# Kernel tuning notes

Measured on AMD Instinct MI355X. Metric: run time of the kernel, lower is better.

The kernel has to match this reference:

```python
import jax, jax.numpy as jnp
import numpy as np

C = 256; CM = 8; MAXI = 100; NCLS = 80
KP = (CM + 2) * CM + CM + CM * CM + CM + CM + 1  # 169 dynamic-kernel params

def _ln(x, g, b, eps=1e-5):
    m = x.mean(-1, keepdims=True)
    v = ((x - m) ** 2).mean(-1, keepdims=True)
    return g * (x - m) * jax.lax.rsqrt(v + eps) + b

def _mlp(x, hw, hb, lng, lnb, fw, fb):
    # torchvision MLP: [Linear -> LayerNorm -> SiLU] * n_hidden -> Linear
    for i in range(hw.shape[0]):
        x = jax.nn.silu(_ln(x @ hw[i] + hb[i], lng[i], lnb[i]))
    return x @ fw + fb

def _conv1x1_bn(x, w, s, b):
    # 1x1 conv (no bias) + inference-mode BatchNorm folded into per-channel affine
    y = jnp.einsum('bchw,oc->bohw', x, w)
    return y * s[None, :, None, None] + b[None, :, None, None]

def _grid(h, w):
    # normalized cell-center coordinates, (x, y) order, shape [h, w, 2]
    ys = (jnp.arange(h, dtype=jnp.float32) + 0.5) / h
    xs = (jnp.arange(w, dtype=jnp.float32) + 0.5) / w
    return jnp.stack([jnp.broadcast_to(xs[None, :], (h, w)),
                      jnp.broadcast_to(ys[:, None], (h, w))], axis=-1)

def setup_inputs() -> dict:
    key = jax.random.key(0)
    ks = iter(jax.random.split(key, 40))
    nrm = lambda shape, s=0.02: s * jax.random.normal(next(ks), shape, jnp.float32)
    B = 4
    inp = {
        'x0': jax.random.normal(next(ks), (B, 3, 512, 512), jnp.float32),
        'x1': jax.random.normal(next(ks), (B, 64, 256, 256), jnp.float32),
        'x2': jax.random.normal(next(ks), (B, 128, 128, 128), jnp.float32),
        'x3': jax.random.normal(next(ks), (B, 256, 64, 64), jnp.float32),
        'x4': jax.random.normal(next(ks), (B, 512, 32, 32), jnp.float32),
        'x5': jax.random.normal(next(ks), (B, 1024, 16, 16), jnp.float32),
        'lat3_w': nrm((C, 256)), 'lat3_s': jnp.ones((C,)), 'lat3_b': jnp.zeros((C,)),
        'lat4_w': nrm((C, 512)), 'lat4_s': jnp.ones((C,)), 'lat4_b': jnp.zeros((C,)),
        'lat5_w': nrm((C, 1024)), 'lat5_s': jnp.ones((C,)), 'lat5_b': jnp.zeros((C,)),
        'mlat_w': nrm((C, 256)), 'mlat_s': jnp.ones((C,)), 'mlat_b': jnp.zeros((C,)),
        'mhead_w': nrm((CM, C, 3, 3)), 'mhead_s': jnp.ones((CM,)), 'mhead_b': jnp.zeros((CM,)),
        'loc_hw': nrm((4, C, C)), 'loc_hb': jnp.zeros((4, C)), 'loc_lng': jnp.ones((4, C)), 'loc_lnb': jnp.zeros((4, C)),
        'loc_fw': nrm((C, 1)), 'loc_fb': -5.0 * jnp.ones((1,)),
        'cls_hw': nrm((4, C, C)), 'cls_hb': jnp.zeros((4, C)), 'cls_lng': jnp.ones((4, C)), 'cls_lnb': jnp.zeros((4, C)),
        'cls_fw': nrm((C, NCLS)), 'cls_fb': jnp.zeros((NCLS,)),
        'ker_hw': nrm((4, C, C)), 'ker_hb': jnp.zeros((4, C)), 'ker_lng': jnp.ones((4, C)), 'ker_lnb': jnp.zeros((4, C)),
        'ker_fw': nrm((C, KP)), 'ker_fb': jnp.zeros((KP,)),
    }
    return inp

def reference(x0, x1, x2, x3, x4, x5,
              lat3_w, lat3_s, lat3_b, lat4_w, lat4_s, lat4_b, lat5_w, lat5_s, lat5_b,
              mlat_w, mlat_s, mlat_b, mhead_w, mhead_s, mhead_b,
              loc_hw, loc_hb, loc_lng, loc_lnb, loc_fw, loc_fb,
              cls_hw, cls_hb, cls_lng, cls_lnb, cls_fw, cls_fb,
              ker_hw, ker_hb, ker_lng, ker_lnb, ker_fw, ker_fb):
    B, _, H, W = x0.shape
    lvls = [(x3, lat3_w, lat3_s, lat3_b), (x4, lat4_w, lat4_s, lat4_b), (x5, lat5_w, lat5_s, lat5_b)]
    feats = [_conv1x1_bn(x, w, s, b) for (x, w, s, b) in lvls]
    flat = jnp.concatenate([f.reshape(B, C, -1).transpose(0, 2, 1) for f in feats], axis=1)  # [B, L, C]
    loc_logits = _mlp(flat, loc_hw, loc_hb, loc_lng, loc_lnb, loc_fw, loc_fb)[..., 0]       # [B, L]
    top_vals, top_idx = jax.lax.top_k(loc_logits, MAXI)
    scores = jax.nn.sigmoid(top_vals)
    num_instances = (scores > 0.5).sum(axis=1)
    gfeat = jnp.take_along_axis(flat, top_idx[:, :, None], axis=1)  # [B, I, C]
    # mask branch
    mf = _conv1x1_bn(x3, mlat_w, mlat_s, mlat_b)
    mf = jax.lax.conv_general_dilated(mf, mhead_w, (1, 1), 'SAME', dimension_numbers=('NCHW', 'OIHW', 'NCHW'))
    mf = jax.nn.silu(mf * mhead_s[None, :, None, None] + mhead_b[None, :, None, None])  # [B, CM, h3, w3]
    h3, w3 = x3.shape[2], x3.shape[3]
    offs_flat = jnp.concatenate([_grid(x.shape[2], x.shape[3]).reshape(-1, 2) for x in (x3, x4, x5)], axis=0)
    offs = offs_flat[top_idx]                                # [B, I, 2]
    grid = _grid(h3, w3).transpose(2, 0, 1)                  # [2, h3, w3]
    grid = grid[None, None] - offs[:, :, :, None, None]      # [B, I, 2, h, w]
    mfi = jnp.broadcast_to(mf[:, None], (B, MAXI, CM, h3, w3))
    feats_i = jnp.concatenate([mfi, grid], axis=2)           # [B, I, CM+2, h, w]
    dyn = _mlp(gfeat, ker_hw, ker_hb, ker_lng, ker_lnb, ker_fw, ker_fb)  # [B, I, KP]
    c = CM
    o = (c + 2) * c
    w1 = dyn[..., :o].reshape(B, MAXI, c + 2, c)
    b1 = dyn[..., o:o + c].reshape(B, MAXI, c, 1, 1); o += c
    w2 = dyn[..., o:o + c * c].reshape(B, MAXI, c, c); o += c * c
    b2 = dyn[..., o:o + c].reshape(B, MAXI, c, 1, 1); o += c
    w3 = dyn[..., o:o + c].reshape(B, MAXI, c, 1); o += c
    b3 = dyn[..., o:].reshape(B, MAXI, 1, 1, 1)
    m = jax.nn.silu(jnp.einsum('bichw,bicd->bidhw', feats_i, w1) + b1)
    m = jax.nn.silu(jnp.einsum('bichw,bicd->bidhw', m, w2) + b2)
    m = jnp.einsum('bichw,bicd->bidhw', m, w3) + b3
    masks = jax.nn.sigmoid(m[:, :, 0])                       # [B, I, h3, w3]
    classes = jnp.argmax(_mlp(gfeat, cls_hw, cls_hb, cls_lng, cls_lnb, cls_fw, cls_fb), axis=-1)
    masks = jax.image.resize(masks, (B, MAXI, H, W), method='bilinear', antialias=False)
    return (num_instances, scores, classes, masks)
```

## Files before the change

kernel.cpp:

```cpp
#include <hip/hip_runtime.h>
#include <hip/hip_bf16.h>
#include <math.h>

#define DEVI __device__ __forceinline__

constexpr int LTOT  = 5376;
constexpr int NINST = 100;
constexpr int NCLS  = 80;
constexpr int KPAR  = 169;

DEVI float waveAllSum(float v) {
#pragma unroll
  for (int s = 32; s > 0; s >>= 1) v += __shfl_xor(v, s, 64);
  return v;
}
DEVI float siluf(float x) { return x / (1.0f + expf(-x)); }
DEVI float sigmf(float x) { return 1.0f / (1.0f + expf(-x)); }

__global__ __launch_bounds__(256) void wtrans(
    const float* __restrict__ w3, const float* __restrict__ w4,
    const float* __restrict__ w5, const float* __restrict__ wm,
    float* __restrict__ wt3, float* __restrict__ wt4,
    float* __restrict__ wt5, float* __restrict__ wtm)
{
  __shared__ float t[64][65];
  const int bid = blockIdx.x;
  const float* src; float* dst; int K, rel;
  if (bid < 16)       { src = w3; dst = wt3; K = 256;  rel = bid; }
  else if (bid < 48)  { src = w4; dst = wt4; K = 512;  rel = bid - 16; }
  else if (bid < 112) { src = w5; dst = wt5; K = 1024; rel = bid - 48; }
  else                { src = wm; dst = wtm; K = 256;  rel = bid - 112; }
  const int ctiles = K >> 6;
  const int ot = rel / ctiles, ct = rel % ctiles;
  const int o0 = ot * 64, c0 = ct * 64;
  const int tid = threadIdx.x;
#pragma unroll
  for (int s = 0; s < 16; ++s) {
    const int e = tid + 256*s;
    const int r = e >> 6, c = e & 63;
    t[r][c] = src[(long)(o0 + r)*K + c0 + c];
  }
  __syncthreads();
#pragma unroll
  for (int s = 0; s < 16; ++s) {
    const int e = tid + 256*s;
    const int q = e >> 6, p = e & 63;
    dst[(long)(c0 + q)*256 + o0 + p] = t[p][q];
  }
}

__global__ __launch_bounds__(256) void lateral_main(
    const float* __restrict__ x3, const float* __restrict__ x4, const float* __restrict__ x5,
    const float* __restrict__ wt3, const float* __restrict__ s3, const float* __restrict__ b3,
    const float* __restrict__ wt4, const float* __restrict__ s4, const float* __restrict__ b4,
    const float* __restrict__ wt5, const float* __restrict__ s5, const float* __restrict__ b5,
    const float* __restrict__ wtm, const float* __restrict__ sm, const float* __restrict__ bm,
    float* __restrict__ flat, float* __restrict__ mlatb)
{
  __shared__ float xs[32][36];
  __shared__ float ws[32][256];
  const int tid = threadIdx.x;
  const int rg = tid >> 6, cg = tid & 63;
  const int bid = blockIdx.x;
  const float *x, *wt, *sc, *bi;
  int K, P, b, p0, baseL = 0; bool tomlat = false;
  if (bid < 512)       { x=x3; wt=wt3; sc=s3; bi=b3; K=256;  P=4096; b=bid>>7;  p0=(bid&127)*32; }
  else if (bid < 1024) { const int rel=bid-512;  x=x3; wt=wtm; sc=sm; bi=bm; K=256;  P=4096; b=rel>>7; p0=(rel&127)*32; tomlat=true; }
  else if (bid < 1152) { const int rel=bid-1024; x=x4; wt=wt4; sc=s4; bi=b4; K=512;  P=1024; b=rel>>5; p0=(rel&31)*32; baseL=4096; }
  else                 { const int rel=bid-1152; x=x5; wt=wt5; sc=s5; bi=b5; K=1024; P=256;  b=rel>>3; p0=(rel&7)*32;  baseL=5120; }
  const float* xb = x + (long)b * K * P;
  float acc[8][4] = {};
  const int nkb = K >> 5;
  for (int kb = 0; kb < nkb; ++kb) {
    __syncthreads();
#pragma unroll
    for (int s = 0; s < 4; ++s) {
      const int e = tid + 256*s;
      const int kk = e >> 5, px = e & 31;
      xs[kk][px] = xb[(long)(kb*32 + kk)*P + p0 + px];
    }
    {
      const float4* w4p = reinterpret_cast<const float4*>(wt + (kb << 13));
#pragma unroll
      for (int q = 0; q < 8; ++q) {
        const int c = tid + (q << 8);
        *reinterpret_cast<float4*>(&ws[c >> 6][4*(c & 63)]) = w4p[c];
      }
    }
    __syncthreads();
#pragma unroll
    for (int kk = 0; kk < 32; ++kk) {
      const float4 a0 = *reinterpret_cast<const float4*>(&xs[kk][8*rg]);
      const float4 a1 = *reinterpret_cast<const float4*>(&xs[kk][8*rg+4]);
      const float ar[8] = {a0.x,a0.y,a0.z,a0.w,a1.x,a1.y,a1.z,a1.w};
      const float4 wv = *reinterpret_cast<const float4*>(&ws[kk][4*cg]);
#pragma unroll
      for (int i = 0; i < 8; ++i) {
        acc[i][0] += ar[i]*wv.x; acc[i][1] += ar[i]*wv.y;
        acc[i][2] += ar[i]*wv.z; acc[i][3] += ar[i]*wv.w;
      }
    }
  }
  const float4 sA = *reinterpret_cast<const float4*>(&sc[4*cg]);
  const float4 bA = *reinterpret_cast<const float4*>(&bi[4*cg]);
  if (!tomlat) {
#pragma unroll
    for (int i = 0; i < 8; ++i) {
      const float4 ov = { acc[i][0]*sA.x+bA.x, acc[i][1]*sA.y+bA.y,
                          acc[i][2]*sA.z+bA.z, acc[i][3]*sA.w+bA.w };
      *reinterpret_cast<float4*>(&flat[((long)b*LTOT + baseL + p0 + 8*rg + i)*256 + 4*cg]) = ov;
    }
  } else {
#pragma unroll
    for (int j = 0; j < 4; ++j) {
      const float sj = (&sA.x)[j], bj = (&bA.x)[j];
      const float4 o0 = { acc[0][j]*sj+bj, acc[1][j]*sj+bj, acc[2][j]*sj+bj, acc[3][j]*sj+bj };
      const float4 o1 = { acc[4][j]*sj+bj, acc[5][j]*sj+bj, acc[6][j]*sj+bj, acc[7][j]*sj+bj };
      float* mb = &mlatb[((long)b*256 + 4*cg + j)*4096 + p0 + 8*rg];
      *reinterpret_cast<float4*>(mb) = o0;
      *reinterpret_cast<float4*>(mb + 4) = o1;
    }
  }
}

__global__ __launch_bounds__(256) void loc4(
    const float* __restrict__ in, const float* __restrict__ hw,
    const float* __restrict__ hb, const float* __restrict__ lng, const float* __restrict__ lnb,
    const float* __restrict__ fw, const float* __restrict__ fb, float* __restrict__ logits)
{
  __shared__ float xs[256][36];
  __shared__ float wsm[16][256];
  const int tid = threadIdx.x;
  const int rg = tid >> 6, cg = tid & 63;
  const long r0 = (long)blockIdx.x * 32;
#pragma unroll
  for (int s = 0; s < 8; ++s) {
    const int e = tid + 256*s;
    const int row = e >> 6, q = e & 63;
    const float4 v = *reinterpret_cast<const float4*>(&in[(r0 + row)*256 + 4*q]);
    const int pc = 8*((row >> 3) ^ (q & 3)) + (row & 7);
#pragma unroll
    for (int j = 0; j < 4; ++j) xs[4*q+j][pc] = (&v.x)[j];
  }
  float ov[8][4];
  for (int L = 0; L < 4; ++L) {
    const float* w = hw + L*65536;
    float acc[8][4] = {};
    for (int kb = 0; kb < 16; ++kb) {
      __syncthreads();
      const float4* w4 = reinterpret_cast<const float4*>(w + (kb << 12));
#pragma unroll
      for (int q = 0; q < 4; ++q) {
        const int c = tid + (q << 8);
        *reinterpret_cast<float4*>(&wsm[c>>6][4*(c&63)]) = w4[c];
      }
      __syncthreads();
#pragma unroll
      for (int kk = 0; kk < 16; ++kk) {
        const int k = (kb << 4) + kk;
        const int col = 8*(rg ^ ((k >> 2) & 3));
        const float4 a0 = *reinterpret_cast<const float4*>(&xs[k][col]);
        const float4 a1 = *reinterpret_cast<const float4*>(&xs[k][col+4]);
        const float4 wv = *reinterpret_cast<const float4*>(&wsm[kk][4*cg]);
        const float ar[8] = {a0.x,a0.y,a0.z,a0.w,a1.x,a1.y,a1.z,a1.w};
#pragma unroll
        for (int i = 0; i < 8; ++i) {
          acc[i][0] += ar[i]*wv.x; acc[i][1] += ar[i]*wv.y;
          acc[i][2] += ar[i]*wv.z; acc[i][3] += ar[i]*wv.w;
        }
      }
    }
    const float4 hb4 = *reinterpret_cast<const float4*>(&hb[L*256 + 4*cg]);
    const float4 g4  = *reinterpret_cast<const float4*>(&lng[L*256 + 4*cg]);
    const float4 lb4 = *reinterpret_cast<const float4*>(&lnb[L*256 + 4*cg]);
#pragma unroll
    for (int i = 0; i < 8; ++i) {
      const float y0 = acc[i][0]+hb4.x, y1 = acc[i][1]+hb4.y;
      const float y2 = acc[i][2]+hb4.z, y3 = acc[i][3]+hb4.w;
      const float m = waveAllSum(y0+y1+y2+y3) * (1.0f/256.0f);
      const float d0=y0-m, d1=y1-m, d2=y2-m, d3=y3-m;
      const float var = waveAllSum(d0*d0+d1*d1+d2*d2+d3*d3) * (1.0f/256.0f);
      const float rs = rsqrtf(var + 1e-5f);
      ov[i][0] = siluf(g4.x*d0*rs + lb4.x);
      ov[i][1] = siluf(g4.y*d1*rs + lb4.y);
      ov[i][2] = siluf(g4.z*d2*rs + lb4.z);
      ov[i][3] = siluf(g4.w*d3*rs + lb4.w);
    }
    __syncthreads();
    if (L < 3) {
      const int colb = 8*(rg ^ (cg & 3));
#pragma unroll
      for (int j = 0; j < 4; ++j) {
        const float4 t0 = {ov[0][j], ov[1][j], ov[2][j], ov[3][j]};
        const float4 t1 = {ov[4][j], ov[5][j], ov[6][j], ov[7][j]};
        *reinterpret_cast<float4*>(&xs[4*cg+j][colb])   = t0;
        *reinterpret_cast<float4*>(&xs[4*cg+j][colb+4]) = t1;
      }
    }
  }
  const float4 fw4 = *reinterpret_cast<const float4*>(&fw[4*cg]);
  const float fbv = fb[0];
#pragma unroll
  for (int i = 0; i < 8; ++i) {
    float d = ov[i][0]*fw4.x + ov[i][1]*fw4.y + ov[i][2]*fw4.z + ov[i][3]*fw4.w;
    d = waveAllSum(d);
    if (cg == 0) logits[r0 + 8*rg + i] = d + fbv;
  }
}

__global__ __launch_bounds__(256) void topk_gather(
    const float* __restrict__ logits, const float* __restrict__ flat,
    int* __restrict__ topi, float* __restrict__ gfeat,
    float* __restrict__ dout)
{
  __shared__ float sv[LTOT];
  __shared__ float rv[4];
  __shared__ int   ri[4];
  __shared__ int   sidx[NINST];
  const int b = blockIdx.x, tid = threadIdx.x;
  for (int l = tid; l < LTOT; l += 256) sv[l] = logits[b*LTOT + l];
  __syncthreads();
  int cnt = 0;
  for (int t = 0; t < NINST; ++t) {
    float bv = -INFINITY; int bidx = 0x7fffffff;
    for (int l = tid; l < LTOT; l += 256) {
      const float v = sv[l];
      if (v > bv) { bv = v; bidx = l; }
    }
#pragma unroll
    for (int s = 32; s > 0; s >>= 1) {
      const float v2 = __shfl_xor(bv, s, 64);
      const int   i2 = __shfl_xor(bidx, s, 64);
      if (v2 > bv || (v2 == bv && i2 < bidx)) { bv = v2; bidx = i2; }
    }
    if ((tid & 63) == 0) { rv[tid >> 6] = bv; ri[tid >> 6] = bidx; }
    __syncthreads();
    if (tid == 0) {
      bv = rv[0]; bidx = ri[0];
#pragma unroll
      for (int q = 1; q < 4; ++q)
        if (rv[q] > bv || (rv[q] == bv && ri[q] < bidx)) { bv = rv[q]; bidx = ri[q]; }
      sidx[t] = bidx; topi[b*NINST + t] = bidx;
      dout[4 + b*NINST + t] = sigmf(bv);
      if (bv > 0.0f) ++cnt;
      sv[bidx] = -INFINITY;
    }
    __syncthreads();
  }
  if (tid == 0) dout[b] = (float)cnt;
  for (int t = 0; t < NINST; ++t) {
    const int ix = sidx[t];
    gfeat[((long)b*NINST + t)*256 + tid] = flat[((long)b*LTOT + ix)*256 + tid];
  }
}

__global__ __launch_bounds__(256) void clsker4(
    const float* __restrict__ gfeat, float* __restrict__ h2,
    const float* __restrict__ chw, const float* __restrict__ chb,
    const float* __restrict__ cg_, const float* __restrict__ cb_,
    const float* __restrict__ khw, const float* __restrict__ khb,
    const float* __restrict__ kg_, const float* __restrict__ kb_)
{
  __shared__ float xs[256][12];
  __shared__ float wsm[16][256];
  const int tid = threadIdx.x;
  const int rg = tid >> 6, cg = tid & 63;
  const bool ker = blockIdx.x >= 50;
  const int r0 = (ker ? (blockIdx.x - 50) : blockIdx.x) * 8;
  const int outr0 = r0 + (ker ? 400 : 0);
  const float* hw = ker ? khw : chw;
  const float* hb = ker ? khb : chb;
  const float* g_ = ker ? kg_ : cg_;
  const float* lb = ker ? kb_ : cb_;
#pragma unroll
  for (int s = 0; s < 2; ++s) {
    const int e = tid + 256*s;
    const int row = e >> 6, q = e & 63;
    const float4 v = *reinterpret_cast<const float4*>(&gfeat[(long)(r0 + row)*256 + 4*q]);
    const int pc = 2*((row >> 1) ^ (q & 3)) + (row & 1);
#pragma unroll
    for (int j = 0; j < 4; ++j) xs[4*q+j][pc] = (&v.x)[j];
  }
  float ov[2][4];
  for (int L = 0; L < 4; ++L) {
    const float* w = hw + L*65536;
    float acc[2][4] = {};
    for (int kb = 0; kb < 16; ++kb) {
      __syncthreads();
      const float4* w4 = reinterpret_cast<const float4*>(w + (kb << 12));
#pragma unroll
      for (int q = 0; q < 4; ++q) {
        const int c = tid + (q << 8);
        *reinterpret_cast<float4*>(&wsm[c>>6][4*(c&63)]) = w4[c];
      }
      __syncthreads();
#pragma unroll
      for (int kk = 0; kk < 16; ++kk) {
        const int k = (kb << 4) + kk;
        const float2 av = *reinterpret_cast<const float2*>(&xs[k][2*(rg ^ ((k >> 2) & 3))]);
        const float4 wv = *reinterpret_cast<const float4*>(&wsm[kk][4*cg]);
        acc[0][0] += av.x*wv.x; acc[0][1] += av.x*wv.y; acc[0][2] += av.x*wv.z; acc[0][3] += av.x*wv.w;
        acc[1][0] += av.y*wv.x; acc[1][1] += av.y*wv.y; acc[1][2] += av.y*wv.z; acc[1][3] += av.y*wv.w;
      }
    }
    const float4 hb4 = *reinterpret_cast<const float4*>(&hb[L*256 + 4*cg]);
    const float4 g4  = *reinterpret_cast<const float4*>(&g_[L*256 + 4*cg]);
    const float4 lb4 = *reinterpret_cast<const float4*>(&lb[L*256 + 4*cg]);
#pragma unroll
    for (int i = 0; i < 2; ++i) {
      const float y0 = acc[i][0]+hb4.x, y1 = acc[i][1]+hb4.y;
      const float y2 = acc[i][2]+hb4.z, y3 = acc[i][3]+hb4.w;
      const float m = waveAllSum(y0+y1+y2+y3) * (1.0f/256.0f);
      const float d0=y0-m, d1=y1-m, d2=y2-m, d3=y3-m;
      const float var = waveAllSum(d0*d0+d1*d1+d2*d2+d3*d3) * (1.0f/256.0f);
      const float rs = rsqrtf(var + 1e-5f);
      ov[i][0] = siluf(g4.x*d0*rs + lb4.x);
      ov[i][1] = siluf(g4.y*d1*rs + lb4.y);
      ov[i][2] = siluf(g4.z*d2*rs + lb4.z);
      ov[i][3] = siluf(g4.w*d3*rs + lb4.w);
    }
    __syncthreads();
    if (L < 3) {
      const int pc = 2*(rg ^ (cg & 3));
#pragma unroll
      for (int j = 0; j < 4; ++j) {
        const float2 t = {ov[0][j], ov[1][j]};
        *reinterpret_cast<float2*>(&xs[4*cg+j][pc]) = t;
      }
    }
  }
#pragma unroll
  for (int i = 0; i < 2; ++i) {
    const float4 o = {ov[i][0], ov[i][1], ov[i][2], ov[i][3]};
    *reinterpret_cast<float4*>(&h2[(long)(outr0 + 2*rg + i)*256 + 4*cg]) = o;
  }
}

__global__ __launch_bounds__(256) void heads(
    const float* __restrict__ h2, const float* __restrict__ cfw, const float* __restrict__ cfb,
    const float* __restrict__ kfw, const float* __restrict__ kfb,
    float* __restrict__ dout, float* __restrict__ dyn)
{
  __shared__ float xr[256];
  __shared__ float lv[NCLS];
  const int bid = blockIdx.x, tid = threadIdx.x;
  xr[tid] = h2[(long)bid*256 + tid];
  __syncthreads();
  if (bid < 400) {
    if (tid < NCLS) {
      float a0=0.f, a1=0.f, a2=0.f, a3=0.f;
      for (int k = 0; k < 256; k += 4) {
        a0 += xr[k+0]*cfw[(k+0)*NCLS + tid];
        a1 += xr[k+1]*cfw[(k+1)*NCLS + tid];
        a2 += xr[k+2]*cfw[(k+2)*NCLS + tid];
        a3 += xr[k+3]*cfw[(k+3)*NCLS + tid];
      }
      lv[tid] = (a0+a1) + (a2+a3) + cfb[tid];
    }
    __syncthreads();
    if (tid == 0) {
      float bv = lv[0]; int bi2 = 0;
      for (int o = 1; o < NCLS; ++o) if (lv[o] > bv) { bv = lv[o]; bi2 = o; }
      dout[404 + bid] = (float)bi2;
    }
  } else {
    if (tid < KPAR) {
      float a0=0.f, a1=0.f, a2=0.f, a3=0.f;
      for (int k = 0; k < 256; k += 4) {
        a0 += xr[k+0]*kfw[(k+0)*KPAR + tid];
        a1 += xr[k+1]*kfw[(k+1)*KPAR + tid];
        a2 += xr[k+2]*kfw[(k+2)*KPAR + tid];
        a3 += xr[k+3]*kfw[(k+3)*KPAR + tid];
      }
      dyn[(long)(bid-400)*KPAR + tid] = (a0+a1) + (a2+a3) + kfb[tid];
    }
  }
}

__global__ __launch_bounds__(256) void conv3(
    const float* __restrict__ mlat, const float* __restrict__ mw,
    float* __restrict__ partial)
{
  const int bid = blockIdx.x;
  const int cc = bid & 7;
  const int tile = (bid >> 3) & 15;
  const int b = bid >> 7;
  const int y0 = (tile >> 2)*16, x0 = (tile & 3)*16;
  const int tid = threadIdx.x;
  const int ly = tid >> 4, lx = tid & 15;
  __shared__ float til[2][18][19];
  __shared__ float wch[8][32][12];
  for (int e = tid; e < 2304; e += 256) {
    const int o = e / 288, rem = e % 288;
    const int c = rem / 9, qq = rem - c*9;
    wch[o][c][qq] = mw[((o*256) + cc*32 + c)*9 + qq];
  }
  int lofs[3], gofs[3], chn[3]; bool vld[3], has[3];
  float* tf = &til[0][0][0];
#pragma unroll
  for (int s = 0; s < 3; ++s) {
    const int e = tid + 256*s;
    has[s] = (e < 648);
    lofs[s] = 0; gofs[s] = 0; chn[s] = 0; vld[s] = false;
    if (has[s]) {
      const int ch = (e >= 324) ? 1 : 0;
      const int pos = e - ch*324;
      const int iy = pos / 18, ix = pos - iy*18;
      const int gy = y0 - 1 + iy, gx = x0 - 1 + ix;
      vld[s] = (gy >= 0 && gy < 64 && gx >= 0 && gx < 64);
      lofs[s] = ch*342 + iy*19 + ix;
      gofs[s] = gy*64 + gx;
      chn[s] = ch;
    }
  }
  const float* xbase = mlat + ((long)b*256 + cc*32)*4096;
  float acc[8] = {};
  for (int r = 0; r < 16; ++r) {
    __syncthreads();
#pragma unroll
    for (int s = 0; s < 3; ++s)
      if (has[s]) tf[lofs[s]] = vld[s] ? xbase[(long)(2*r + chn[s])*4096 + gofs[s]] : 0.f;
    __syncthreads();
#pragma unroll
    for (int ch = 0; ch < 2; ++ch) {
      const int c = 2*r + ch;
      float t[9];
#pragma unroll
      for (int dy = 0; dy < 3; ++dy)
#pragma unroll
        for (int dx = 0; dx < 3; ++dx) t[dy*3+dx] = til[ch][ly+dy][lx+dx];
#pragma unroll
      for (int o = 0; o < 8; ++o) {
        const float4 wa = *reinterpret_cast<const float4*>(&wch[o][c][0]);
        const float4 wb = *reinterpret_cast<const float4*>(&wch[o][c][4]);
        const float w8 = wch[o][c][8];
        acc[o] += t[0]*wa.x + t[1]*wa.y + t[2]*wa.z + t[3]*wa.w
                + t[4]*wb.x + t[5]*wb.y + t[6]*wb.z + t[7]*wb.w + t[8]*w8;
      }
    }
  }
  const long pbase = (((long)b*8 + cc)*8)*4096 + (y0+ly)*64 + (x0+lx);
#pragma unroll
  for (int o = 0; o < 8; ++o) partial[pbase + (long)o*4096] = acc[o];
}

__global__ __launch_bounds__(256) void mhead_fin(
    const float* __restrict__ partial, const float* __restrict__ s,
    const float* __restrict__ bi, float* __restrict__ mhead)
{
  const int idx = blockIdx.x*256 + threadIdx.x;
  const int p = idx & 4095;
  const int o = (idx >> 12) & 7;
  const int b = idx >> 15;
  float v = 0.f;
#pragma unroll
  for (int cc = 0; cc < 8; ++cc) v += partial[(((long)b*8 + cc)*8 + o)*4096 + p];
  v = v*s[o] + bi[o];
  mhead[idx] = siluf(v);
}

__global__ __launch_bounds__(256) void mask_fused(
    const float* __restrict__ dyn, const int* __restrict__ topi,
    const float* __restrict__ mhead, float* __restrict__ dout)
{
  __shared__ float msrc[18][64];
  __shared__ float dd[KPAR];
  __shared__ float so[2];
  const int bid = blockIdx.x;
  const int inst = bid >> 2, q = bid & 3;
  const int tid = threadIdx.x;
  if (tid < KPAR) dd[tid] = dyn[(long)inst*KPAR + tid];
  if (tid == 0) {
    const int l = topi[inst];
    float ox, oy;
    if (l < 4096)      { ox = ((l & 63) + 0.5f)*(1.f/64.f); oy = ((l >> 6) + 0.5f)*(1.f/64.f); }
    else if (l < 5120) { const int t = l - 4096; ox = ((t & 31) + 0.5f)*(1.f/32.f); oy = ((t >> 5) + 0.5f)*(1.f/32.f); }
    else               { const int t = l - 5120; ox = ((t & 15) + 0.5f)*(1.f/16.f); oy = ((t >> 4) + 0.5f)*(1.f/16.f); }
    so[0] = ox; so[1] = oy;
  }
  __syncthreads();
  const float ox = so[0], oy = so[1];
  const int b = inst / NINST;
  const float* mh = mhead + (long)b*8*4096;
  const int r0s = 16*q - 1;
  for (int e = tid; e < 1152; e += 256) {
    const int r = e >> 6, x = e & 63;
    int sy = r0s + r; sy = sy < 0 ? 0 : (sy > 63 ? 63 : sy);
    const int p = sy*64 + x;
    float f[10];
#pragma unroll
    for (int c = 0; c < 8; ++c) f[c] = mh[c*4096 + p];
    f[8] = (x + 0.5f)*(1.f/64.f) - ox;
    f[9] = (sy + 0.5f)*(1.f/64.f) - oy;
    float m1[8];
#pragma unroll
    for (int d = 0; d < 8; ++d) {
      float t = dd[80 + d];
#pragma unroll
      for (int c = 0; c < 10; ++c) t += f[c]*dd[c*8 + d];
      m1[d] = siluf(t);
    }
    float m2[8];
#pragma unroll
    for (int d = 0; d < 8; ++d) {
      float t = dd[152 + d];
#pragma unroll
      for (int c = 0; c < 8; ++c) t += m1[c]*dd[88 + c*8 + d];
      m2[d] = siluf(t);
    }
    float o = dd[168];
#pragma unroll
    for (int c = 0; c < 8; ++c) o += m2[c]*dd[160 + c];
    msrc[r][x] = sigmf(o);
  }
  __syncthreads();
  const int j4 = tid & 127;
  const int half = tid >> 7;
  const int ix0 = (j4 & 1) ? (j4 >> 1) : (j4 >> 1) - 1;
  const int xlo = ix0 < 0 ? 0 : ix0;
  const int xhi = (ix0 + 1 > 63) ? 63 : ix0 + 1;
  float fx[4];
#pragma unroll
  for (int m = 0; m < 4; ++m) {
    const int x = 4*j4 + m;
    const float tx = (x + 0.5f)*0.125f - 0.5f;
    fx[m] = tx - (float)ix0;
  }
  float* dbase = dout + 804 + ((long)inst << 18);
  for (int it = 0; it < 64; ++it) {
    const int yy = 2*it + half;
    const int y = 128*q + yy;
    const float ty = (y + 0.5f)*0.125f - 0.5f;
    const float fyf = floorf(ty);
    const int iy0 = (int)fyf;
    const float fy = ty - fyf;
    const int r0 = iy0 - r0s;
    const float L0 = msrc[r0][xlo],   R0 = msrc[r0][xhi];
    const float L1 = msrc[r0+1][xlo], R1 = msrc[r0+1][xhi];
    const float L = L0 + (L1 - L0)*fy;
    const float R = R0 + (R1 - R0)*fy;
    const float4 ovv = { L + (R - L)*fx[0], L + (R - L)*fx[1],
                         L + (R - L)*fx[2], L + (R - L)*fx[3] };
    *reinterpret_cast<float4*>(&dbase[((long)y << 9) + (j4 << 2)]) = ovv;
  }
}

extern "C" void kernel_launch(void* const* d_in, const int* in_sizes, int n_in,
                              void* d_out, int out_size, void* d_ws, size_t ws_size,
                              hipStream_t stream)
{
  (void)in_sizes; (void)n_in; (void)out_size; (void)ws_size;
  const float* x3      = (const float*)d_in[3];
  const float* x4      = (const float*)d_in[4];
  const float* x5      = (const float*)d_in[5];
  const float* lat3_w  = (const float*)d_in[6];
  const float* lat3_s  = (const float*)d_in[7];
  const float* lat3_b  = (const float*)d_in[8];
  const float* lat4_w  = (const float*)d_in[9];
  const float* lat4_s  = (const float*)d_in[10];
  const float* lat4_b  = (const float*)d_in[11];
  const float* lat5_w  = (const float*)d_in[12];
  const float* lat5_s  = (const float*)d_in[13];
  const float* lat5_b  = (const float*)d_in[14];
  const float* mlat_w  = (const float*)d_in[15];
  const float* mlat_s  = (const float*)d_in[16];
  const float* mlat_b  = (const float*)d_in[17];
  const float* mhead_w = (const float*)d_in[18];
  const float* mhead_s = (const float*)d_in[19];
  const float* mhead_b = (const float*)d_in[20];
  const float* loc_hw  = (const float*)d_in[21];
  const float* loc_hb  = (const float*)d_in[22];
  const float* loc_lng = (const float*)d_in[23];
  const float* loc_lnb = (const float*)d_in[24];
  const float* loc_fw  = (const float*)d_in[25];
  const float* loc_fb  = (const float*)d_in[26];
  const float* cls_hw  = (const float*)d_in[27];
  const float* cls_hb  = (const float*)d_in[28];
  const float* cls_lng = (const float*)d_in[29];
  const float* cls_lnb = (const float*)d_in[30];
  const float* cls_fw  = (const float*)d_in[31];
  const float* cls_fb  = (const float*)d_in[32];
  const float* ker_hw  = (const float*)d_in[33];
  const float* ker_hb  = (const float*)d_in[34];
  const float* ker_lng = (const float*)d_in[35];
  const float* ker_lnb = (const float*)d_in[36];
  const float* ker_fw  = (const float*)d_in[37];
  const float* ker_fb  = (const float*)d_in[38];

  float* ws      = (float*)d_ws;
  float* flat    = ws;
  float* mlatb   = ws + 5505024;
  float* partial = ws + 9699328;
  float* mheadb  = ws + 10747904;
  float* h2      = ws + 10878976;
  float* logits  = ws + 11083776;
  int*   topi    = (int*)(ws + 11105280);
  float* gfeat   = ws + 11105680;
  float* dynb    = ws + 11208080;
  float* wt3     = ws + 11275680;
  float* wt4     = ws + 11341216;
  float* wt5     = ws + 11472288;
  float* wtm     = ws + 11734432;
  float* dout    = (float*)d_out;

  wtrans<<<128, 256, 0, stream>>>(lat3_w, lat4_w, lat5_w, mlat_w, wt3, wt4, wt5, wtm);
  lateral_main<<<1184, 256, 0, stream>>>(x3, x4, x5,
      wt3, lat3_s, lat3_b, wt4, lat4_s, lat4_b, wt5, lat5_s, lat5_b,
      wtm, mlat_s, mlat_b, flat, mlatb);
  conv3<<<512, 256, 0, stream>>>(mlatb, mhead_w, partial);
  mhead_fin<<<512, 256, 0, stream>>>(partial, mhead_s, mhead_b, mheadb);
  loc4<<<672, 256, 0, stream>>>(flat, loc_hw, loc_hb, loc_lng, loc_lnb,
                                loc_fw, loc_fb, logits);
  topk_gather<<<4, 256, 0, stream>>>(logits, flat, topi, gfeat, dout);
  clsker4<<<100, 256, 0, stream>>>(gfeat, h2,
      cls_hw, cls_hb, cls_lng, cls_lnb, ker_hw, ker_hb, ker_lng, ker_lnb);
  heads<<<800, 256, 0, stream>>>(h2, cls_fw, cls_fb, ker_fw, ker_fb, dout, dynb);
  mask_fused<<<1600, 256, 0, stream>>>(dynb, topi, mheadb, dout);
}
```

Before: 888.8 us.

## Keep loc MLP activations in registers, broadcast via readlane, double-buffer weights

The loc4 MLP kernel now keeps each row's activations in registers across layers and broadcasts each k-element with readlane. This replaces the shared-memory activation tile and its transposed write-back between layers. Weight tiles are double-buffered in LDS, with the next tile prefetched into registers while the current one is consumed, which cuts the barriers to one per k-block. Rows per block drop from 32 to 16 and the grid doubles, so there is more parallelism, but each weight load is reused across half as many rows and global weight traffic doubles.

```diff
diff --git a/kernel.cpp b/kernel.cpp
--- a/kernel.cpp
+++ b/kernel.cpp
@@ -16,6 +16,9 @@
 }
 DEVI float siluf(float x) { return x / (1.0f + expf(-x)); }
 DEVI float sigmf(float x) { return 1.0f / (1.0f + expf(-x)); }
+DEVI float rdlane(float v, int lane) {
+  return __int_as_float(__builtin_amdgcn_readlane(__float_as_int(v), lane));
+}
 
 __global__ __launch_bounds__(256) void wtrans(
     const float* __restrict__ w3, const float* __restrict__ w4,
@@ -128,83 +131,82 @@
     const float* __restrict__ hb, const float* __restrict__ lng, const float* __restrict__ lnb,
     const float* __restrict__ fw, const float* __restrict__ fb, float* __restrict__ logits)
 {
-  __shared__ float xs[256][36];
-  __shared__ float wsm[16][256];
+  __shared__ float wsm[2][16][256];
   const int tid = threadIdx.x;
   const int rg = tid >> 6, cg = tid & 63;
-  const long r0 = (long)blockIdx.x * 32;
-#pragma unroll
-  for (int s = 0; s < 8; ++s) {
-    const int e = tid + 256*s;
-    const int row = e >> 6, q = e & 63;
-    const float4 v = *reinterpret_cast<const float4*>(&in[(r0 + row)*256 + 4*q]);
-    const int pc = 8*((row >> 3) ^ (q & 3)) + (row & 7);
-#pragma unroll
-    for (int j = 0; j < 4; ++j) xs[4*q+j][pc] = (&v.x)[j];
-  }
-  float ov[8][4];
+  const long r0 = (long)blockIdx.x * 16;
+  float xv[4][4];
+#pragma unroll
+  for (int i = 0; i < 4; ++i) {
+    const float4 v = *reinterpret_cast<const float4*>(&in[(r0 + 4*rg + i)*256 + 4*cg]);
+    xv[i][0]=v.x; xv[i][1]=v.y; xv[i][2]=v.z; xv[i][3]=v.w;
+  }
+  float4 wpre[4];
+  {
+    const float4* w4p = reinterpret_cast<const float4*>(hw);
+#pragma unroll
+    for (int q = 0; q < 4; ++q) wpre[q] = w4p[tid + (q << 8)];
+#pragma unroll
+    for (int q = 0; q < 4; ++q) {
+      const int c = tid + (q << 8);
+      *reinterpret_cast<float4*>(&wsm[0][c >> 6][4*(c & 63)]) = wpre[q];
+    }
+    __syncthreads();
+  }
   for (int L = 0; L < 4; ++L) {
-    const float* w = hw + L*65536;
-    float acc[8][4] = {};
+    float acc[4][4] = {};
     for (int kb = 0; kb < 16; ++kb) {
+      const int g = (L << 4) + kb;
+      const int cur = g & 1;
+      if (g + 1 < 64) {
+        const float4* w4p = reinterpret_cast<const float4*>(hw + ((long)(g + 1) << 12));
+#pragma unroll
+        for (int q = 0; q < 4; ++q) wpre[q] = w4p[tid + (q << 8)];
+      }
+#pragma unroll
+      for (int kk = 0; kk < 16; ++kk) {
+        const float4 wv = *reinterpret_cast<const float4*>(&wsm[cur][kk][4*cg]);
+        const int lanek = (kb << 2) + (kk >> 2);
+#pragma unroll
+        for (int i = 0; i < 4; ++i) {
+          const float a = rdlane(xv[i][kk & 3], lanek);
+          acc[i][0] += a*wv.x; acc[i][1] += a*wv.y;
+          acc[i][2] += a*wv.z; acc[i][3] += a*wv.w;
+        }
+      }
+      if (g + 1 < 64) {
+#pragma unroll
+        for (int q = 0; q < 4; ++q) {
+          const int c = tid + (q << 8);
+          *reinterpret_cast<float4*>(&wsm[cur ^ 1][c >> 6][4*(c & 63)]) = wpre[q];
+        }
+      }
       __syncthreads();
-      const float4* w4 = reinterpret_cast<const float4*>(w + (kb << 12));
-#pragma unroll
-      for (int q = 0; q < 4; ++q) {
-        const int c = tid + (q << 8);
-        *reinterpret_cast<float4*>(&wsm[c>>6][4*(c&63)]) = w4[c];
-      }
-      __syncthreads();
-#pragma unroll
-      for (int kk = 0; kk < 16; ++kk) {
-        const int k = (kb << 4) + kk;
-        const int col = 8*(rg ^ ((k >> 2) & 3));
-        const float4 a0 = *reinterpret_cast<const float4*>(&xs[k][col]);
-        const float4 a1 = *reinterpret_cast<const float4*>(&xs[k][col+4]);
-        const float4 wv = *reinterpret_cast<const float4*>(&wsm[kk][4*cg]);
-        const float ar[8] = {a0.x,a0.y,a0.z,a0.w,a1.x,a1.y,a1.z,a1.w};
-#pragma unroll
-        for (int i = 0; i < 8; ++i) {
-          acc[i][0] += ar[i]*wv.x; acc[i][1] += ar[i]*wv.y;
-          acc[i][2] += ar[i]*wv.z; acc[i][3] += ar[i]*wv.w;
-        }
-      }
     }
     const float4 hb4 = *reinterpret_cast<const float4*>(&hb[L*256 + 4*cg]);
     const float4 g4  = *reinterpret_cast<const float4*>(&lng[L*256 + 4*cg]);
     const float4 lb4 = *reinterpret_cast<const float4*>(&lnb[L*256 + 4*cg]);
 #pragma unroll
-    for (int i = 0; i < 8; ++i) {
+    for (int i = 0; i < 4; ++i) {
       const float y0 = acc[i][0]+hb4.x, y1 = acc[i][1]+hb4.y;
       const float y2 = acc[i][2]+hb4.z, y3 = acc[i][3]+hb4.w;
       const float m = waveAllSum(y0+y1+y2+y3) * (1.0f/256.0f);
       const float d0=y0-m, d1=y1-m, d2=y2-m, d3=y3-m;
       const float var = waveAllSum(d0*d0+d1*d1+d2*d2+d3*d3) * (1.0f/256.0f);
       const float rs = rsqrtf(var + 1e-5f);
-      ov[i][0] = siluf(g4.x*d0*rs + lb4.x);
-      ov[i][1] = siluf(g4.y*d1*rs + lb4.y);
-      ov[i][2] = siluf(g4.z*d2*rs + lb4.z);
-      ov[i][3] = siluf(g4.w*d3*rs + lb4.w);
-    }
-    __syncthreads();
-    if (L < 3) {
-      const int colb = 8*(rg ^ (cg & 3));
-#pragma unroll
-      for (int j = 0; j < 4; ++j) {
-        const float4 t0 = {ov[0][j], ov[1][j], ov[2][j], ov[3][j]};
-        const float4 t1 = {ov[4][j], ov[5][j], ov[6][j], ov[7][j]};
-        *reinterpret_cast<float4*>(&xs[4*cg+j][colb])   = t0;
-        *reinterpret_cast<float4*>(&xs[4*cg+j][colb+4]) = t1;
-      }
+      xv[i][0] = siluf(g4.x*d0*rs + lb4.x);
+      xv[i][1] = siluf(g4.y*d1*rs + lb4.y);
+      xv[i][2] = siluf(g4.z*d2*rs + lb4.z);
+      xv[i][3] = siluf(g4.w*d3*rs + lb4.w);
     }
   }
   const float4 fw4 = *reinterpret_cast<const float4*>(&fw[4*cg]);
   const float fbv = fb[0];
 #pragma unroll
-  for (int i = 0; i < 8; ++i) {
-    float d = ov[i][0]*fw4.x + ov[i][1]*fw4.y + ov[i][2]*fw4.z + ov[i][3]*fw4.w;
+  for (int i = 0; i < 4; ++i) {
+    float d = xv[i][0]*fw4.x + xv[i][1]*fw4.y + xv[i][2]*fw4.z + xv[i][3]*fw4.w;
     d = waveAllSum(d);
-    if (cg == 0) logits[r0 + 8*rg + i] = d + fbv;
+    if (cg == 0) logits[r0 + 4*rg + i] = d + fbv;
   }
 }
 
@@ -609,8 +611,8 @@
       wtm, mlat_s, mlat_b, flat, mlatb);
   conv3<<<512, 256, 0, stream>>>(mlatb, mhead_w, partial);
   mhead_fin<<<512, 256, 0, stream>>>(partial, mhead_s, mhead_b, mheadb);
-  loc4<<<672, 256, 0, stream>>>(flat, loc_hw, loc_hb, loc_lng, loc_lnb,
-                                loc_fw, loc_fb, logits);
+  loc4<<<1344, 256, 0, stream>>>(flat, loc_hw, loc_hb, loc_lng, loc_lnb,
+                                 loc_fw, loc_fb, logits);
   topk_gather<<<4, 256, 0, stream>>>(logits, flat, topi, gfeat, dout);
   clsker4<<<100, 256, 0, stream>>>(gfeat, h2,
       cls_hw, cls_hb, cls_lng, cls_lnb, ker_hw, ker_hb, ker_lng, ker_lnb);
```

After: 1.020 ms. 1.15x slower.
